# Performance work log

Hardware: AMD Instinct MI355X
Metric: run time of the kernel (lower is better)

## Reference

```python
import jax, jax.numpy as jnp
import numpy as np

B, L, H = 2, 2048, 1024
NH, KVH = 16, 4
HD = H // NH          # 64
G = NH // KVH         # 4 query heads per kv head


def setup_inputs() -> dict:
    key = jax.random.key(0)
    ks = jax.random.split(key, 10)
    s = 0.02
    return {
        "hidden_states": jax.random.normal(ks[0], (B, L, H), dtype=jnp.float32),
        "attention_mask": jnp.zeros((B, 1, L, L), dtype=jnp.float32),
        "Wq": jax.random.normal(ks[1], (H, H), dtype=jnp.float32) * s,
        "bq": jnp.zeros((H,), dtype=jnp.float32),
        "Wk": jax.random.normal(ks[2], (KVH * HD, H), dtype=jnp.float32) * s,
        "bk": jnp.zeros((KVH * HD,), dtype=jnp.float32),
        "Wv": jax.random.normal(ks[3], (KVH * HD, H), dtype=jnp.float32) * s,
        "bv": jnp.zeros((KVH * HD,), dtype=jnp.float32),
        "Wo": jax.random.normal(ks[4], (H, H), dtype=jnp.float32) * s,
        "bo": jnp.zeros((H,), dtype=jnp.float32),
    }


def reference(hidden_states, attention_mask, Wq, bq, Wk, bk, Wv, bv, Wo, bo):
    x = hidden_states
    # projections (torch Linear: x @ W.T + b)
    q = (x @ Wq.T + bq).reshape(B, L, NH, HD).transpose(0, 2, 1, 3)   # [B,NH,L,HD]
    k = (x @ Wk.T + bk).reshape(B, L, KVH, HD).transpose(0, 2, 1, 3)  # [B,KVH,L,HD]
    v = (x @ Wv.T + bv).reshape(B, L, KVH, HD).transpose(0, 2, 1, 3)
    # GQA: group query heads per kv head instead of repeat_interleave (same math)
    qg = q.reshape(B, KVH, G, L, HD)
    scores = jnp.einsum("bkgqd,bkld->bkgql", qg, k) / jnp.sqrt(jnp.float32(HD))
    scores = scores + attention_mask[:, :, None, :, :]  # mask broadcasts over heads
    attn = jax.nn.softmax(scores, axis=-1)              # dropout p=0 -> identity
    ctx = jnp.einsum("bkgql,bkld->bkgqd", attn, v)      # [B,KVH,G,L,HD]
    ctx = ctx.reshape(B, NH, L, HD).transpose(0, 2, 1, 3).reshape(B, L, H)
    return ctx @ Wo.T + bo
```

## Files before the change

kernel.cpp:

```cpp
#include <hip/hip_runtime.h>

#define B_   2
#define L_   2048
#define H_   1024
#define NH_  16
#define KVH_ 4
#define HD_  64

typedef short short8 __attribute__((ext_vector_type(8)));
typedef float f32x4 __attribute__((ext_vector_type(4)));
typedef float f32x16 __attribute__((ext_vector_type(16)));
typedef unsigned short u16x4 __attribute__((ext_vector_type(4)));

#define LOG2E 1.4426950408889634f
#define QSC   0.18033688011112042f
#define MFMA   __builtin_amdgcn_mfma_f32_16x16x32_bf16
#define MFMA32 __builtin_amdgcn_mfma_f32_32x32x16_bf16

#if __has_builtin(__builtin_amdgcn_exp2f)
#define EXP2(x) __builtin_amdgcn_exp2f(x)
#else
#define EXP2(x) exp2f(x)
#endif

static __device__ __forceinline__ unsigned short f2bf(float f) {
  unsigned int u = __float_as_uint(f);
  u += 0x7FFFu + ((u >> 16) & 1u);
  return (unsigned short)(u >> 16);
}

static __device__ __forceinline__ unsigned int cvtpk(float lo, float hi) {
  unsigned int r;
  asm("v_cvt_pk_bf16_f32 %0, %1, %2" : "=v"(r) : "v"(lo), "v"(hi));
  return r;
}

static __device__ __forceinline__ void plswap(unsigned int& a, unsigned int& b) {
  asm("v_permlane32_swap_b32 %0, %1" : "+v"(a), "+v"(b));
}

static __device__ __forceinline__ short8 mk8(unsigned int w0, unsigned int w1,
                                             unsigned int w2, unsigned int w3) {
  union { unsigned int u[4]; short8 s; } x;
  x.u[0] = w0; x.u[1] = w1; x.u[2] = w2; x.u[3] = w3;
  return x.s;
}

static __device__ __forceinline__ void gload_lds16(const void* g, void* l) {
  __builtin_amdgcn_global_load_lds(
      (const __attribute__((address_space(1))) unsigned int*)g,
      (__attribute__((address_space(3))) unsigned int*)l, 16, 0, 0);
}

__global__ __launch_bounds__(256) void k_prep(const float* __restrict__ x,
                                              const float* __restrict__ Wq,
                                              const float* __restrict__ Wk,
                                              const float* __restrict__ Wv,
                                              const float* __restrict__ Wo,
                                              const float* __restrict__ mask,
                                              unsigned short* __restrict__ xb,
                                              unsigned short* __restrict__ wcat,
                                              unsigned short* __restrict__ wo_b,
                                              unsigned char* __restrict__ flags) {
  const int blk = blockIdx.x;
  const int t = threadIdx.x;
  if (blk < 4096) {
    size_t i = ((size_t)blk * 256 + t) * 4;
    float4 v = *(const float4*)(x + i);
    u16x4 o = { f2bf(v.x), f2bf(v.y), f2bf(v.z), f2bf(v.w) };
    *(u16x4*)(xb + i) = o;
  } else if (blk < 6656) {
    int r = blk - 4096;
    int c = t * 4;
    const float* src;
    unsigned short* dst;
    if (r < 1024)      { src = Wq + (size_t)r * 1024;          dst = wcat + (size_t)r * 1024; }
    else if (r < 1280) { src = Wk + (size_t)(r - 1024) * 1024; dst = wcat + (size_t)r * 1024; }
    else if (r < 1536) { src = Wv + (size_t)(r - 1280) * 1024; dst = wcat + (size_t)r * 1024; }
    else               { src = Wo + (size_t)(r - 1536) * 1024; dst = wo_b + (size_t)(r - 1536) * 1024; }
    float4 v = *(const float4*)(src + c);
    u16x4 o = { f2bf(v.x), f2bf(v.y), f2bf(v.z), f2bf(v.w) };
    *(u16x4*)(dst + c) = o;
  } else {
    const int mb = blk - 6656;
    const int b = mb >> 10, qb = (mb >> 5) & 31, kb = mb & 31;
    const float* base = mask + ((size_t)b * L_ + qb * 64) * L_ + kb * 64;
    const int r0 = t >> 4, c = (t & 15) * 4;
    bool nz = false;
#pragma unroll
    for (int i = 0; i < 4; ++i) {
      float4 v = *(const float4*)(base + (size_t)(r0 + i * 16) * L_ + c);
      nz |= (v.x != 0.f) | (v.y != 0.f) | (v.z != 0.f) | (v.w != 0.f);
    }
    __shared__ int anyv;
    if (t == 0) anyv = 0;
    __syncthreads();
    if (__any(nz) && (t & 63) == 0) atomicOr(&anyv, 1);
    __syncthreads();
    if (t == 0) flags[mb] = (unsigned char)anyv;
  }
}

template <int MODE>
__global__ __launch_bounds__(256) void k_gemm(const unsigned short* __restrict__ A,
                                              const unsigned short* __restrict__ Bt,
                                              const float* __restrict__ bias0,
                                              const float* __restrict__ bias1,
                                              const float* __restrict__ bias2,
                                              unsigned short* __restrict__ q_ws,
                                              unsigned short* __restrict__ k_ws,
                                              unsigned short* __restrict__ vt_ws,
                                              float* __restrict__ outp) {
  const int bn = blockIdx.x, bm = blockIdx.y;
  const int t = threadIdx.x;
  const int lane = t & 63, li = lane & 15, g = lane >> 4;
  const int wid = t >> 6, wr = wid >> 1, wc = wid & 1;
  __shared__ unsigned short lds_a[128 * 32];
  __shared__ unsigned short lds_b[128 * 32];

  const f32x4 z = {0.f, 0.f, 0.f, 0.f};
  f32x4 acc[4][4];
#pragma unroll
  for (int m = 0; m < 4; ++m)
#pragma unroll
    for (int n = 0; n < 4; ++n) acc[m][n] = z;

  const int c0 = t, c1 = 256 + t;
  const int r0 = c0 >> 2, o0 = (c0 & 3) * 8;
  const int r1 = c1 >> 2, o1 = (c1 & 3) * 8;
  const unsigned short* a0p = A + (size_t)(bm * 128 + r0) * 1024 + o0;
  const unsigned short* a1p = A + (size_t)(bm * 128 + r1) * 1024 + o1;
  const unsigned short* b0p = Bt + (size_t)(bn * 128 + r0) * 1024 + o0;
  const unsigned short* b1p = Bt + (size_t)(bn * 128 + r1) * 1024 + o1;

  for (int kt = 0; kt < 1024; kt += 32) {
    gload_lds16(a0p + kt, &lds_a[c0 * 8]);
    gload_lds16(a1p + kt, &lds_a[c1 * 8]);
    gload_lds16(b0p + kt, &lds_b[c0 * 8]);
    gload_lds16(b1p + kt, &lds_b[c1 * 8]);
    __syncthreads();
    short8 af[4], bf[4];
#pragma unroll
    for (int m = 0; m < 4; ++m) af[m] = *(const short8*)&lds_a[(wr * 64 + m * 16 + li) * 32 + g * 8];
#pragma unroll
    for (int n = 0; n < 4; ++n) bf[n] = *(const short8*)&lds_b[(wc * 64 + n * 16 + li) * 32 + g * 8];
#pragma unroll
    for (int m = 0; m < 4; ++m)
#pragma unroll
      for (int n = 0; n < 4; ++n)
        acc[m][n] = MFMA(af[m], bf[n], acc[m][n], 0, 0, 0);
    __syncthreads();
  }

#pragma unroll
  for (int m = 0; m < 4; ++m) {
    const int row0 = bm * 128 + wr * 64 + m * 16 + 4 * g;
#pragma unroll
    for (int n = 0; n < 4; ++n) {
      const int col = bn * 128 + wc * 64 + n * 16 + li;
      f32x4 v = acc[m][n];
      if (MODE == 1) {
        const float bias = bias0[col];
#pragma unroll
        for (int r = 0; r < 4; ++r) outp[(size_t)(row0 + r) * 1024 + col] = v[r] + bias;
      } else {
        if (col < 1024) {
          const float bias = bias0[col];
#pragma unroll
          for (int r = 0; r < 4; ++r) q_ws[(size_t)(row0 + r) * 1024 + col] = f2bf((v[r] + bias) * QSC);
        } else if (col < 1280) {
          const int cc = col - 1024;
          const float bias = bias1[cc];
#pragma unroll
          for (int r = 0; r < 4; ++r) k_ws[(size_t)(row0 + r) * 256 + cc] = f2bf(v[r] + bias);
        } else {
          const int cc = col - 1280;
          const float bias = bias2[cc];
          const int kvh = cc >> 6, d = cc & 63;
          const int b = row0 >> 11, l0 = row0 & 2047;
          u16x4 pk = { f2bf(v[0] + bias), f2bf(v[1] + bias), f2bf(v[2] + bias), f2bf(v[3] + bias) };
          *(u16x4*)(vt_ws + ((size_t)((b * KVH_ + kvh) * 64 + d)) * 2048 + l0) = pk;
        }
      }
    }
  }
}

__global__ __launch_bounds__(256, 2) void k_attn(const unsigned short* __restrict__ q_ws,
                                                 const unsigned short* __restrict__ k_ws,
                                                 const unsigned short* __restrict__ vt_ws,
                                                 const float* __restrict__ mask,
                                                 const unsigned char* __restrict__ mflags,
                                                 unsigned short* __restrict__ ctx) {
  const int bk = blockIdx.x;
  const int qt = blockIdx.y;
  const int b = bk >> 2, kvh = bk & 3;
  const int t = threadIdx.x;
  const int wid = t >> 6, lane = t & 63;
  const int l31 = lane & 31, g1 = lane >> 5;
  const int kh = wid >> 1, hp = wid & 1;

  __shared__ unsigned short smem[16384];
  __shared__ float lred[2][2][64];

  const unsigned short* qbase = q_ws + ((size_t)b * L_ + qt * 32 + l31) * H_ +
                                (kvh * 4 + hp * 2) * 64 + g1 * 8;
  short8 qf[2][4];
#pragma unroll
  for (int h2 = 0; h2 < 2; ++h2)
#pragma unroll
    for (int ks = 0; ks < 4; ++ks)
      qf[h2][ks] = *(const short8*)(qbase + h2 * 64 + ks * 16);

  const unsigned int* fp = (const unsigned int*)(mflags + b * 1024 + (qt >> 1) * 32);
  unsigned int fm = 0;
#pragma unroll
  for (int w = 0; w < 8; ++w) {
    unsigned int wv = fp[w];
    fm |= ((wv & 0x000000FFu) ? 1u : 0u) << (w * 4 + 0);
    fm |= ((wv & 0x0000FF00u) ? 1u : 0u) << (w * 4 + 1);
    fm |= ((wv & 0x00FF0000u) ? 1u : 0u) << (w * 4 + 2);
    fm |= ((wv & 0xFF000000u) ? 1u : 0u) << (w * 4 + 3);
  }
  fm = __builtin_amdgcn_readfirstlane(fm);

  const int srow = t >> 3, sgr = t & 7;
  const int swz = (sgr ^ (srow & 7)) * 8;
  const unsigned short* ksrc = k_ws + ((size_t)b * L_ + srow) * 256 + kvh * 64 + swz;
  const unsigned short* vsrc = vt_ws + ((size_t)(b * KVH_ + kvh) * 64 + srow) * 2048 + swz;

  f32x16 o_[4];
  const f32x16 z16 = {0,0,0,0,0,0,0,0,0,0,0,0,0,0,0,0};
#pragma unroll
  for (int i = 0; i < 4; ++i) o_[i] = z16;
  float l_part[2] = {0.f, 0.f};

  const int rK = kh * 32 + l31, swK = rK & 7;
  const int rV0 = l31, rV1 = 32 + l31;
  const int swV0 = rV0 & 7, swV1 = rV1 & 7;

#define STAGE(buf, kt)                                                        \
  {                                                                           \
    unsigned short* dk = smem + (buf) * 8192;                                 \
    unsigned short* dv = dk + 4096;                                           \
    _Pragma("unroll")                                                         \
    for (int i = 0; i < 2; ++i) {                                             \
      gload_lds16(ksrc + ((size_t)(kt) * 64 + i * 32) * 256, dk + (t + 256 * i) * 8); \
      gload_lds16(vsrc + (size_t)i * 32 * 2048 + (kt) * 64,  dv + (t + 256 * i) * 8); \
    }                                                                         \
  }

  STAGE(0, 0);
  __syncthreads();

#pragma unroll 1
  for (int kt = 0; kt < 32; ++kt) {
    const int cur = kt & 1;
    if (kt + 1 < 32) STAGE(cur ^ 1, kt + 1);

    const unsigned short* lk = smem + cur * 8192;
    const unsigned short* lv = lk + 4096;

    short8 kf[4];
#pragma unroll
    for (int ks = 0; ks < 4; ++ks)
      kf[ks] = *(const short8*)&lk[rK * 64 + ((ks * 2 + g1) ^ swK) * 8];
    short8 vf[2][2];
#pragma unroll
    for (int s = 0; s < 2; ++s) {
      vf[0][s] = *(const short8*)&lv[rV0 * 64 + ((kh * 4 + s * 2 + g1) ^ swV0) * 8];
      vf[1][s] = *(const short8*)&lv[rV1 * 64 + ((kh * 4 + s * 2 + g1) ^ swV1) * 8];
    }

    f32x16 sv[2];
    sv[0] = z16; sv[1] = z16;
    __builtin_amdgcn_s_setprio(1);
#pragma unroll
    for (int ks = 0; ks < 4; ++ks) sv[0] = MFMA32(kf[ks], qf[0][ks], sv[0], 0, 0, 0);
#pragma unroll
    for (int ks = 0; ks < 4; ++ks) sv[1] = MFMA32(kf[ks], qf[1][ks], sv[1], 0, 0, 0);
    __builtin_amdgcn_s_setprio(0);

    if (fm & (1u << kt)) {
      const float* mrow = mask + ((size_t)b * L_ + qt * 32 + l31) * L_ + kt * 64 + kh * 32 + g1 * 4;
#pragma unroll
      for (int rg = 0; rg < 4; ++rg) {
        float4 mv = *(const float4*)(mrow + rg * 8);
#pragma unroll
        for (int j = 0; j < 4; ++j) {
          const float mj = (&mv.x)[j] * LOG2E;
          sv[0][rg * 4 + j] += mj;
          sv[1][rg * 4 + j] += mj;
        }
      }
    }

    short8 pa[2][2];
#pragma unroll
    for (int h2 = 0; h2 < 2; ++h2) {
      float e[16];
#pragma unroll
      for (int r = 0; r < 16; ++r) e[r] = EXP2(sv[h2][r]);
      l_part[h2] += (((e[0] + e[1]) + (e[2] + e[3])) + ((e[4] + e[5]) + (e[6] + e[7]))) +
                    (((e[8] + e[9]) + (e[10] + e[11])) + ((e[12] + e[13]) + (e[14] + e[15])));
      unsigned int w0 = cvtpk(e[0], e[1]),   w1 = cvtpk(e[2], e[3]);
      unsigned int w2 = cvtpk(e[4], e[5]),   w3 = cvtpk(e[6], e[7]);
      unsigned int w4 = cvtpk(e[8], e[9]),   w5 = cvtpk(e[10], e[11]);
      unsigned int w6 = cvtpk(e[12], e[13]), w7 = cvtpk(e[14], e[15]);
      plswap(w0, w2); plswap(w1, w3);
      plswap(w4, w6); plswap(w5, w7);
      pa[h2][0] = mk8(w0, w1, w2, w3);
      pa[h2][1] = mk8(w4, w5, w6, w7);
    }

    __builtin_amdgcn_s_setprio(1);
#pragma unroll
    for (int h2 = 0; h2 < 2; ++h2)
#pragma unroll
      for (int db = 0; db < 2; ++db) {
        o_[h2 * 2 + db] = MFMA32(vf[db][0], pa[h2][0], o_[h2 * 2 + db], 0, 0, 0);
        o_[h2 * 2 + db] = MFMA32(vf[db][1], pa[h2][1], o_[h2 * 2 + db], 0, 0, 0);
      }
    __builtin_amdgcn_s_setprio(0);

    __syncthreads();
  }
#undef STAGE

  float lt0 = l_part[0] + __shfl_xor(l_part[0], 32);
  float lt1 = l_part[1] + __shfl_xor(l_part[1], 32);
  float* red = (float*)smem;

  if (kh == 1) {
    lred[hp][0][lane] = lt0;
    lred[hp][1][lane] = lt1;
#pragma unroll
    for (int db = 0; db < 2; ++db)
#pragma unroll
      for (int w4 = 0; w4 < 4; ++w4) {
        f32x4 pv = { o_[db][w4 * 4 + 0], o_[db][w4 * 4 + 1],
                     o_[db][w4 * 4 + 2], o_[db][w4 * 4 + 3] };
        *(f32x4*)&red[(((w4 * 2 + hp) * 2 + db) * 64 + lane) * 4] = pv;
      }
  }
  __syncthreads();

  if (kh == 0) {
    const float inv = 1.f / (lt0 + lred[hp][0][lane]);
#pragma unroll
    for (int db = 0; db < 2; ++db) {
      f32x16 acc = o_[db];
#pragma unroll
      for (int w4 = 0; w4 < 4; ++w4) {
        f32x4 pv = *(const f32x4*)&red[(((w4 * 2 + hp) * 2 + db) * 64 + lane) * 4];
#pragma unroll
        for (int j = 0; j < 4; ++j) acc[w4 * 4 + j] += pv[j];
      }
      unsigned short* cp = ctx + ((size_t)b * L_ + qt * 32 + l31) * H_ +
                           (kvh * 4 + hp * 2) * 64 + db * 32 + g1 * 4;
#pragma unroll
      for (int k4 = 0; k4 < 4; ++k4) {
        unsigned int a0 = cvtpk(acc[4 * k4 + 0] * inv, acc[4 * k4 + 1] * inv);
        unsigned int a1 = cvtpk(acc[4 * k4 + 2] * inv, acc[4 * k4 + 3] * inv);
        *(unsigned int*)(cp + 8 * k4) = a0;
        *(unsigned int*)(cp + 8 * k4 + 2) = a1;
      }
    }
  }
  __syncthreads();

  if (kh == 1) {
#pragma unroll
    for (int db = 0; db < 2; ++db)
#pragma unroll
      for (int w4 = 0; w4 < 4; ++w4) {
        f32x4 pv = { o_[2 + db][w4 * 4 + 0], o_[2 + db][w4 * 4 + 1],
                     o_[2 + db][w4 * 4 + 2], o_[2 + db][w4 * 4 + 3] };
        *(f32x4*)&red[(((w4 * 2 + hp) * 2 + db) * 64 + lane) * 4] = pv;
      }
  }
  __syncthreads();

  if (kh == 0) {
    const float inv = 1.f / (lt1 + lred[hp][1][lane]);
#pragma unroll
    for (int db = 0; db < 2; ++db) {
      f32x16 acc = o_[2 + db];
#pragma unroll
      for (int w4 = 0; w4 < 4; ++w4) {
        f32x4 pv = *(const f32x4*)&red[(((w4 * 2 + hp) * 2 + db) * 64 + lane) * 4];
#pragma unroll
        for (int j = 0; j < 4; ++j) acc[w4 * 4 + j] += pv[j];
      }
      unsigned short* cp = ctx + ((size_t)b * L_ + qt * 32 + l31) * H_ +
                           (kvh * 4 + hp * 2 + 1) * 64 + db * 32 + g1 * 4;
#pragma unroll
      for (int k4 = 0; k4 < 4; ++k4) {
        unsigned int a0 = cvtpk(acc[4 * k4 + 0] * inv, acc[4 * k4 + 1] * inv);
        unsigned int a1 = cvtpk(acc[4 * k4 + 2] * inv, acc[4 * k4 + 3] * inv);
        *(unsigned int*)(cp + 8 * k4) = a0;
        *(unsigned int*)(cp + 8 * k4 + 2) = a1;
      }
    }
  }
}

extern "C" void kernel_launch(void* const* d_in, const int* in_sizes, int n_in,
                              void* d_out, int out_size, void* d_ws, size_t ws_size,
                              hipStream_t stream) {
  const float* x    = (const float*)d_in[0];
  const float* mask = (const float*)d_in[1];
  const float* Wq   = (const float*)d_in[2];
  const float* bq   = (const float*)d_in[3];
  const float* Wk   = (const float*)d_in[4];
  const float* bk   = (const float*)d_in[5];
  const float* Wv   = (const float*)d_in[6];
  const float* bv   = (const float*)d_in[7];
  const float* Wo   = (const float*)d_in[8];
  const float* bo   = (const float*)d_in[9];
  float* out = (float*)d_out;

  char* ws = (char*)d_ws;
  unsigned short* xb    = (unsigned short*)(ws);
  unsigned short* ctx   = xb;
  unsigned short* wcat  = (unsigned short*)(ws + 8388608);
  unsigned short* wo_b  = (unsigned short*)(ws + 11534336);
  unsigned short* q_ws  = (unsigned short*)(ws + 13631488);
  unsigned short* k_ws  = (unsigned short*)(ws + 22020096);
  unsigned short* vt_ws = (unsigned short*)(ws + 24117248);
  unsigned char*  mflg  = (unsigned char*)(ws + 26214400);

  k_prep<<<dim3(8704), dim3(256), 0, stream>>>(x, Wq, Wk, Wv, Wo, mask, xb, wcat, wo_b, mflg);
  k_gemm<0><<<dim3(12, 32), dim3(256), 0, stream>>>(xb, wcat, bq, bk, bv, q_ws, k_ws, vt_ws, nullptr);
  k_attn<<<dim3(8, 64), dim3(256), 0, stream>>>(q_ws, k_ws, vt_ws, mask, mflg, ctx);
  k_gemm<1><<<dim3(8, 32), dim3(256), 0, stream>>>(ctx, wo_b, bo, nullptr, nullptr,
                                                   nullptr, nullptr, nullptr, out);
}
```

Before: 114.1 us.

## Split attention block into 8 waves, one query head per wave

```diff
diff --git a/kernel.cpp b/kernel.cpp
--- a/kernel.cpp
+++ b/kernel.cpp
@@ -186,7 +186,7 @@
   }
 }
 
-__global__ __launch_bounds__(256, 2) void k_attn(const unsigned short* __restrict__ q_ws,
+__global__ __launch_bounds__(512, 4) void k_attn(const unsigned short* __restrict__ q_ws,
                                                  const unsigned short* __restrict__ k_ws,
                                                  const unsigned short* __restrict__ vt_ws,
                                                  const float* __restrict__ mask,
@@ -198,19 +198,16 @@
   const int t = threadIdx.x;
   const int wid = t >> 6, lane = t & 63;
   const int l31 = lane & 31, g1 = lane >> 5;
-  const int kh = wid >> 1, hp = wid & 1;
+  const int h = wid & 3, kh = wid >> 2;
 
   __shared__ unsigned short smem[16384];
-  __shared__ float lred[2][2][64];
+  __shared__ float lred[4][64];
 
   const unsigned short* qbase = q_ws + ((size_t)b * L_ + qt * 32 + l31) * H_ +
-                                (kvh * 4 + hp * 2) * 64 + g1 * 8;
-  short8 qf[2][4];
-#pragma unroll
-  for (int h2 = 0; h2 < 2; ++h2)
-#pragma unroll
-    for (int ks = 0; ks < 4; ++ks)
-      qf[h2][ks] = *(const short8*)(qbase + h2 * 64 + ks * 16);
+                                (kvh * 4 + h) * 64 + g1 * 8;
+  short8 qf[4];
+#pragma unroll
+  for (int ks = 0; ks < 4; ++ks) qf[ks] = *(const short8*)(qbase + ks * 16);
 
   const unsigned int* fp = (const unsigned int*)(mflags + b * 1024 + (qt >> 1) * 32);
   unsigned int fm = 0;
@@ -229,25 +226,19 @@
   const unsigned short* ksrc = k_ws + ((size_t)b * L_ + srow) * 256 + kvh * 64 + swz;
   const unsigned short* vsrc = vt_ws + ((size_t)(b * KVH_ + kvh) * 64 + srow) * 2048 + swz;
 
-  f32x16 o_[4];
   const f32x16 z16 = {0,0,0,0,0,0,0,0,0,0,0,0,0,0,0,0};
-#pragma unroll
-  for (int i = 0; i < 4; ++i) o_[i] = z16;
-  float l_part[2] = {0.f, 0.f};
+  f32x16 o_[2];
+  o_[0] = z16; o_[1] = z16;
+  float l_part = 0.f;
 
   const int rK = kh * 32 + l31, swK = rK & 7;
-  const int rV0 = l31, rV1 = 32 + l31;
-  const int swV0 = rV0 & 7, swV1 = rV1 & 7;
+  const int swV = l31 & 7;
 
 #define STAGE(buf, kt)                                                        \
   {                                                                           \
     unsigned short* dk = smem + (buf) * 8192;                                 \
-    unsigned short* dv = dk + 4096;                                           \
-    _Pragma("unroll")                                                         \
-    for (int i = 0; i < 2; ++i) {                                             \
-      gload_lds16(ksrc + ((size_t)(kt) * 64 + i * 32) * 256, dk + (t + 256 * i) * 8); \
-      gload_lds16(vsrc + (size_t)i * 32 * 2048 + (kt) * 64,  dv + (t + 256 * i) * 8); \
-    }                                                                         \
+    gload_lds16(ksrc + (size_t)(kt) * 64 * 256, dk + t * 8);                  \
+    gload_lds16(vsrc + (kt) * 64, dk + 4096 + t * 8);                         \
   }
 
   STAGE(0, 0);
@@ -267,18 +258,15 @@
       kf[ks] = *(const short8*)&lk[rK * 64 + ((ks * 2 + g1) ^ swK) * 8];
     short8 vf[2][2];
 #pragma unroll
-    for (int s = 0; s < 2; ++s) {
-      vf[0][s] = *(const short8*)&lv[rV0 * 64 + ((kh * 4 + s * 2 + g1) ^ swV0) * 8];
-      vf[1][s] = *(const short8*)&lv[rV1 * 64 + ((kh * 4 + s * 2 + g1) ^ swV1) * 8];
-    }
-
-    f32x16 sv[2];
-    sv[0] = z16; sv[1] = z16;
+    for (int db = 0; db < 2; ++db)
+#pragma unroll
+      for (int s = 0; s < 2; ++s)
+        vf[db][s] = *(const short8*)&lv[(db * 32 + l31) * 64 + ((kh * 4 + s * 2 + g1) ^ swV) * 8];
+
+    f32x16 sv = z16;
     __builtin_amdgcn_s_setprio(1);
 #pragma unroll
-    for (int ks = 0; ks < 4; ++ks) sv[0] = MFMA32(kf[ks], qf[0][ks], sv[0], 0, 0, 0);
-#pragma unroll
-    for (int ks = 0; ks < 4; ++ks) sv[1] = MFMA32(kf[ks], qf[1][ks], sv[1], 0, 0, 0);
+    for (int ks = 0; ks < 4; ++ks) sv = MFMA32(kf[ks], qf[ks], sv, 0, 0, 0);
     __builtin_amdgcn_s_setprio(0);
 
     if (fm & (1u << kt)) {
@@ -287,113 +275,65 @@
       for (int rg = 0; rg < 4; ++rg) {
         float4 mv = *(const float4*)(mrow + rg * 8);
 #pragma unroll
-        for (int j = 0; j < 4; ++j) {
-          const float mj = (&mv.x)[j] * LOG2E;
-          sv[0][rg * 4 + j] += mj;
-          sv[1][rg * 4 + j] += mj;
-        }
-      }
-    }
-
-    short8 pa[2][2];
-#pragma unroll
-    for (int h2 = 0; h2 < 2; ++h2) {
-      float e[16];
-#pragma unroll
-      for (int r = 0; r < 16; ++r) e[r] = EXP2(sv[h2][r]);
-      l_part[h2] += (((e[0] + e[1]) + (e[2] + e[3])) + ((e[4] + e[5]) + (e[6] + e[7]))) +
-                    (((e[8] + e[9]) + (e[10] + e[11])) + ((e[12] + e[13]) + (e[14] + e[15])));
-      unsigned int w0 = cvtpk(e[0], e[1]),   w1 = cvtpk(e[2], e[3]);
-      unsigned int w2 = cvtpk(e[4], e[5]),   w3 = cvtpk(e[6], e[7]);
-      unsigned int w4 = cvtpk(e[8], e[9]),   w5 = cvtpk(e[10], e[11]);
-      unsigned int w6 = cvtpk(e[12], e[13]), w7 = cvtpk(e[14], e[15]);
-      plswap(w0, w2); plswap(w1, w3);
-      plswap(w4, w6); plswap(w5, w7);
-      pa[h2][0] = mk8(w0, w1, w2, w3);
-      pa[h2][1] = mk8(w4, w5, w6, w7);
-    }
+        for (int j = 0; j < 4; ++j) sv[rg * 4 + j] = fmaf((&mv.x)[j], LOG2E, sv[rg * 4 + j]);
+      }
+    }
+
+    float e[16];
+#pragma unroll
+    for (int r = 0; r < 16; ++r) e[r] = EXP2(sv[r]);
+    l_part += (((e[0] + e[1]) + (e[2] + e[3])) + ((e[4] + e[5]) + (e[6] + e[7]))) +
+              (((e[8] + e[9]) + (e[10] + e[11])) + ((e[12] + e[13]) + (e[14] + e[15])));
+    unsigned int w0 = cvtpk(e[0], e[1]),   w1 = cvtpk(e[2], e[3]);
+    unsigned int w2 = cvtpk(e[4], e[5]),   w3 = cvtpk(e[6], e[7]);
+    unsigned int w4 = cvtpk(e[8], e[9]),   w5 = cvtpk(e[10], e[11]);
+    unsigned int w6 = cvtpk(e[12], e[13]), w7 = cvtpk(e[14], e[15]);
+    plswap(w0, w2); plswap(w1, w3);
+    plswap(w4, w6); plswap(w5, w7);
+    short8 pa0 = mk8(w0, w1, w2, w3);
+    short8 pa1 = mk8(w4, w5, w6, w7);
 
     __builtin_amdgcn_s_setprio(1);
 #pragma unroll
-    for (int h2 = 0; h2 < 2; ++h2)
-#pragma unroll
-      for (int db = 0; db < 2; ++db) {
-        o_[h2 * 2 + db] = MFMA32(vf[db][0], pa[h2][0], o_[h2 * 2 + db], 0, 0, 0);
-        o_[h2 * 2 + db] = MFMA32(vf[db][1], pa[h2][1], o_[h2 * 2 + db], 0, 0, 0);
-      }
+    for (int db = 0; db < 2; ++db) {
+      o_[db] = MFMA32(vf[db][0], pa0, o_[db], 0, 0, 0);
+      o_[db] = MFMA32(vf[db][1], pa1, o_[db], 0, 0, 0);
+    }
     __builtin_amdgcn_s_setprio(0);
 
     __syncthreads();
   }
 #undef STAGE
 
-  float lt0 = l_part[0] + __shfl_xor(l_part[0], 32);
-  float lt1 = l_part[1] + __shfl_xor(l_part[1], 32);
+  float lt = l_part + __shfl_xor(l_part, 32);
   float* red = (float*)smem;
 
   if (kh == 1) {
-    lred[hp][0][lane] = lt0;
-    lred[hp][1][lane] = lt1;
+    lred[h][lane] = lt;
 #pragma unroll
     for (int db = 0; db < 2; ++db)
 #pragma unroll
       for (int w4 = 0; w4 < 4; ++w4) {
         f32x4 pv = { o_[db][w4 * 4 + 0], o_[db][w4 * 4 + 1],
                      o_[db][w4 * 4 + 2], o_[db][w4 * 4 + 3] };
-        *(f32x4*)&red[(((w4 * 2 + hp) * 2 + db) * 64 + lane) * 4] = pv;
+        *(f32x4*)&red[(((h * 2 + db) * 4 + w4) * 64 + lane) * 4] = pv;
       }
   }
   __syncthreads();
 
   if (kh == 0) {
-    const float inv = 1.f / (lt0 + lred[hp][0][lane]);
+    const float inv = 1.f / (lt + lred[h][lane]);
 #pragma unroll
     for (int db = 0; db < 2; ++db) {
       f32x16 acc = o_[db];
 #pragma unroll
       for (int w4 = 0; w4 < 4; ++w4) {
-        f32x4 pv = *(const f32x4*)&red[(((w4 * 2 + hp) * 2 + db) * 64 + lane) * 4];
+        f32x4 pv = *(const f32x4*)&red[(((h * 2 + db) * 4 + w4) * 64 + lane) * 4];
 #pragma unroll
         for (int j = 0; j < 4; ++j) acc[w4 * 4 + j] += pv[j];
       }
       unsigned short* cp = ctx + ((size_t)b * L_ + qt * 32 + l31) * H_ +
-                           (kvh * 4 + hp * 2) * 64 + db * 32 + g1 * 4;
-#pragma unroll
-      for (int k4 = 0; k4 < 4; ++k4) {
-        unsigned int a0 = cvtpk(acc[4 * k4 + 0] * inv, acc[4 * k4 + 1] * inv);
-        unsigned int a1 = cvtpk(acc[4 * k4 + 2] * inv, acc[4 * k4 + 3] * inv);
-        *(unsigned int*)(cp + 8 * k4) = a0;
-        *(unsigned int*)(cp + 8 * k4 + 2) = a1;
-      }
-    }
-  }
-  __syncthreads();
-
-  if (kh == 1) {
-#pragma unroll
-    for (int db = 0; db < 2; ++db)
-#pragma unroll
-      for (int w4 = 0; w4 < 4; ++w4) {
-        f32x4 pv = { o_[2 + db][w4 * 4 + 0], o_[2 + db][w4 * 4 + 1],
-                     o_[2 + db][w4 * 4 + 2], o_[2 + db][w4 * 4 + 3] };
-        *(f32x4*)&red[(((w4 * 2 + hp) * 2 + db) * 64 + lane) * 4] = pv;
-      }
-  }
-  __syncthreads();
-
-  if (kh == 0) {
-    const float inv = 1.f / (lt1 + lred[hp][1][lane]);
-#pragma unroll
-    for (int db = 0; db < 2; ++db) {
-      f32x16 acc = o_[2 + db];
-#pragma unroll
-      for (int w4 = 0; w4 < 4; ++w4) {
-        f32x4 pv = *(const f32x4*)&red[(((w4 * 2 + hp) * 2 + db) * 64 + lane) * 4];
-#pragma unroll
-        for (int j = 0; j < 4; ++j) acc[w4 * 4 + j] += pv[j];
-      }
-      unsigned short* cp = ctx + ((size_t)b * L_ + qt * 32 + l31) * H_ +
-                           (kvh * 4 + hp * 2 + 1) * 64 + db * 32 + g1 * 4;
+                           (kvh * 4 + h) * 64 + db * 32 + g1 * 4;
 #pragma unroll
       for (int k4 = 0; k4 < 4; ++k4) {
         unsigned int a0 = cvtpk(acc[4 * k4 + 0] * inv, acc[4 * k4 + 1] * inv);
@@ -432,7 +372,7 @@
 
   k_prep<<<dim3(8704), dim3(256), 0, stream>>>(x, Wq, Wk, Wv, Wo, mask, xb, wcat, wo_b, mflg);
   k_gemm<0><<<dim3(12, 32), dim3(256), 0, stream>>>(xb, wcat, bq, bk, bv, q_ws, k_ws, vt_ws, nullptr);
-  k_attn<<<dim3(8, 64), dim3(256), 0, stream>>>(q_ws, k_ws, vt_ws, mask, mflg, ctx);
+  k_attn<<<dim3(8, 64), dim3(512), 0, stream>>>(q_ws, k_ws, vt_ws, mask, mflg, ctx);
   k_gemm<1><<<dim3(8, 32), dim3(256), 0, stream>>>(ctx, wo_b, bo, nullptr, nullptr,
                                                    nullptr, nullptr, nullptr, out);
 }
```

Measured after the change: 114.5 us. About the same (+0.3%).
